# Kernel optimization log

Hardware: AMD Instinct MI355X
Metric: run time of the kernel (lower is better)

Reference implementation:

```python
import jax, jax.numpy as jnp
import numpy as np
from functools import partial

INPUT_DIM = 256
HIDDEN = 512
NUM_LAYERS = 2

def _linp(key, fan_in, shape):
    # torch nn.Linear/Conv default init: U(-1/sqrt(fan_in), 1/sqrt(fan_in))
    bound = 1.0 / np.sqrt(fan_in)
    return jax.random.uniform(key, shape, jnp.float32, -bound, bound)

def setup_inputs() -> dict:
    key = jax.random.key(0)
    ks = iter(jax.random.split(key, 64))
    d = {}
    d["x"] = jax.random.normal(next(ks), (32, 16, 1, 64, 64), jnp.float32)
    # encoder convs (OIHW)
    d["conv1_w"] = _linp(next(ks), 1 * 9, (16, 1, 3, 3));   d["conv1_b"] = _linp(next(ks), 1 * 9, (16,))
    d["conv2_w"] = _linp(next(ks), 16 * 9, (32, 16, 3, 3)); d["conv2_b"] = _linp(next(ks), 16 * 9, (32,))
    d["conv3_w"] = _linp(next(ks), 32 * 9, (INPUT_DIM, 32, 3, 3)); d["conv3_b"] = _linp(next(ks), 32 * 9, (INPUT_DIM,))
    # LSTM cells: per layer 4 gate linears (forget, input, cell, output), in = input+hidden
    for j in range(NUM_LAYERS):
        fan = (INPUT_DIM if j == 0 else HIDDEN) + HIDDEN
        for g in ("f", "i", "g", "o"):
            d[f"W{g}{j}"] = _linp(next(ks), fan, (fan, HIDDEN))
            d[f"b{g}{j}"] = _linp(next(ks), fan, (HIDDEN,))
    # classifier
    d["cw1"] = _linp(next(ks), HIDDEN, (HIDDEN, 128)); d["cb1"] = _linp(next(ks), HIDDEN, (128,))
    d["cw2"] = _linp(next(ks), 128, (128, 64));        d["cb2"] = _linp(next(ks), 128, (64,))
    d["cw3"] = _linp(next(ks), 64, (64, 6));           d["cb3"] = _linp(next(ks), 64, (6,))
    return d

def _conv(x, w, b):
    y = jax.lax.conv_general_dilated(x, w, (1, 1), "SAME",
                                     dimension_numbers=("NCHW", "OIHW", "NCHW"))
    return y + b[None, :, None, None]

def _maxpool2(x):
    return jax.lax.reduce_window(x, -jnp.inf, jax.lax.max,
                                 (1, 1, 2, 2), (1, 1, 2, 2), "VALID")

def reference(x, conv1_w, conv1_b, conv2_w, conv2_b, conv3_w, conv3_b,
              Wf0, bf0, Wi0, bi0, Wg0, bg0, Wo0, bo0,
              Wf1, bf1, Wi1, bi1, Wg1, bg1, Wo1, bo1,
              cw1, cb1, cw2, cb2, cw3, cb3):
    B, T, C, H, W = x.shape
    xf = x.reshape(B * T, C, H, W)
    h = _maxpool2(jax.nn.relu(_conv(xf, conv1_w, conv1_b)))
    h = _maxpool2(jax.nn.relu(_conv(h, conv2_w, conv2_b)))
    h = jax.nn.relu(_conv(h, conv3_w, conv3_b))
    emb = h.mean(axis=(2, 3)).reshape(B, T, -1)  # AdaptiveAvgPool2d((1,1)); dropout = identity (eval)

    layers = [(Wf0, bf0, Wi0, bi0, Wg0, bg0, Wo0, bo0),
              (Wf1, bf1, Wi1, bi1, Wg1, bg1, Wo1, bo1)]

    def step(carry, x_t):
        hs, cs = carry
        inp = x_t
        new_h, new_c = [], []
        for j, (Wf, bf, Wi, bi, Wg, bg, Wo, bo) in enumerate(layers):
            comb = jnp.concatenate([inp, hs[j]], axis=1)  # [B, in+H]
            f_t = jax.nn.sigmoid(comb @ Wf + bf)
            i_t = jax.nn.sigmoid(comb @ Wi + bi)
            g_t = jnp.tanh(comb @ Wg + bg)
            o_t = jax.nn.sigmoid(comb @ Wo + bo)
            c_n = f_t * cs[j] + i_t * g_t
            h_n = o_t * jnp.tanh(c_n)
            new_h.append(h_n); new_c.append(c_n)
            inp = h_n
        return (tuple(new_h), tuple(new_c)), None

    h0 = tuple(jnp.zeros((B, HIDDEN), x.dtype) for _ in range(NUM_LAYERS))
    c0 = tuple(jnp.zeros((B, HIDDEN), x.dtype) for _ in range(NUM_LAYERS))
    (hs, _), _ = jax.lax.scan(step, (h0, c0), jnp.swapaxes(emb, 0, 1))
    last = hs[-1]  # [B, HIDDEN], last timestep top-layer h (dropout = identity)

    y = jax.nn.relu(last @ cw1 + cb1)
    y = jax.nn.relu(y @ cw2 + cb2)
    return y @ cw3 + cb3  # [B, 6]
```

## Files before the change

kernel.cpp:

```cpp
#include <hip/hip_runtime.h>
#include <math.h>

__global__ void k_conv1(const float* __restrict__ x, const float* __restrict__ w,
                        const float* __restrict__ bias, float* __restrict__ out) {
  int idx = blockIdx.x * 256 + threadIdx.x;
  int ox = idx & 31, oy = (idx >> 5) & 31, oc = (idx >> 10) & 15, n = idx >> 14;
  const float* im = x + n * 4096;
  float wv[9];
#pragma unroll
  for (int i = 0; i < 9; ++i) wv[i] = w[oc * 9 + i];
  float bs = bias[oc];
  float m = 0.f;
#pragma unroll
  for (int dy = 0; dy < 2; ++dy)
#pragma unroll
    for (int dx = 0; dx < 2; ++dx) {
      int cy = oy * 2 + dy, cx = ox * 2 + dx;
      float s = bs;
#pragma unroll
      for (int ky = 0; ky < 3; ++ky) {
        int yy = cy + ky - 1;
        if (yy < 0 || yy >= 64) continue;
#pragma unroll
        for (int kx = 0; kx < 3; ++kx) {
          int xx = cx + kx - 1;
          if (xx < 0 || xx >= 64) continue;
          s += im[yy * 64 + xx] * wv[ky * 3 + kx];
        }
      }
      m = fmaxf(m, fmaxf(s, 0.f));
    }
  out[idx] = m;
}

__global__ void k_prep_w(const float* __restrict__ w2, float* __restrict__ w2t,
                         const float* __restrict__ w3, float* __restrict__ w3t) {
  int id = blockIdx.x * 256 + threadIdx.x;
  if (id < 73728) {
    int ct = id >> 8, oc = id & 255;
    int c = ct / 9, tap = ct - 9 * c;
    w3t[id] = w3[(oc * 32 + c) * 9 + tap];
  }
  if (id < 4608) {
    int ct = id >> 5, oc = id & 31;
    int c = ct / 9, tap = ct - 9 * c;
    w2t[id] = w2[(oc * 16 + c) * 9 + tap];
  }
}

__global__ __launch_bounds__(256) void k_conv2(
    const float* __restrict__ a1, const float* __restrict__ w2t,
    const float* __restrict__ bias, float* __restrict__ a2) {
  __shared__ __align__(16) float ins[8 * 1024];
  int n = blockIdx.x, ocg = blockIdx.y;
  int tid = threadIdx.x;
  int py = tid >> 4, px = tid & 15;
  int y0 = 2 * py - 1, x0 = 2 * px - 1;
  float acc[16][4] = {};
  const float* wb = w2t + ocg * 16;
  for (int ph = 0; ph < 2; ++ph) {
    __syncthreads();
    const float4* src = (const float4*)(a1 + n * 16384 + ph * 8192);
    for (int i = tid; i < 2048; i += 256) ((float4*)ins)[i] = src[i];
    __syncthreads();
    for (int c = 0; c < 8; ++c) {
      float wv[4][4];
#pragma unroll
      for (int r = 0; r < 4; ++r) {
        int y = y0 + r;
        bool vy = (y >= 0) && (y < 32);
        int yc = vy ? y : 0;
#pragma unroll
        for (int cc = 0; cc < 4; ++cc) {
          int xx = x0 + cc;
          bool vx = (xx >= 0) && (xx < 32);
          int xc = vx ? xx : 0;
          float t = ins[c * 1024 + yc * 32 + xc];
          wv[r][cc] = (vy && vx) ? t : 0.f;
        }
      }
      int ch = ph * 8 + c;
#pragma unroll
      for (int ky = 0; ky < 3; ++ky)
#pragma unroll
        for (int kx = 0; kx < 3; ++kx) {
          const float* w16 = wb + (ch * 9 + ky * 3 + kx) * 32;
#pragma unroll
          for (int i = 0; i < 4; ++i) {
            float vv = wv[(i >> 1) + ky][(i & 1) + kx];
#pragma unroll
            for (int j = 0; j < 16; ++j) acc[j][i] += vv * w16[j];
          }
        }
    }
  }
  const float* bp = bias + ocg * 16;
  float4 o[4];
#pragma unroll
  for (int j = 0; j < 16; ++j) {
    float m = fmaxf(fmaxf(acc[j][0], acc[j][1]), fmaxf(acc[j][2], acc[j][3]));
    ((float*)o)[j] = fmaxf(m + bp[j], 0.f);
  }
  float4* dst = (float4*)(a2 + (size_t)(n * 256 + tid) * 32 + ocg * 16);
#pragma unroll
  for (int q = 0; q < 4; ++q) dst[q] = o[q];
}

__global__ __launch_bounds__(512) void k_conv3(
    const float* __restrict__ a2, const float* __restrict__ w3t,
    const float* __restrict__ bias, float* __restrict__ comb0) {
  __shared__ __align__(16) float ins[324 * 20];
  float4* ins4 = (float4*)ins;
  int n = blockIdx.x, ocb = blockIdx.y;
  int tid = threadIdx.x;
  for (int i = tid; i < 1620; i += 512) ins4[i] = float4{0.f, 0.f, 0.f, 0.f};
  int wvid = __builtin_amdgcn_readfirstlane(tid >> 6);
  int lane = tid & 63;
  int tr = lane >> 4, tc = lane & 15;
  float acc[4][8] = {};
  const float* wbase = w3t + ocb * 64 + wvid * 8;
  const float4* src = (const float4*)(a2 + (size_t)n * 8192);
  for (int hf = 0; hf < 2; ++hf) {
    __syncthreads();
    for (int i = tid; i < 1024; i += 512) {
      int px = i >> 2, cg = i & 3;
      int p = ((px >> 4) + 1) * 18 + (px & 15) + 1;
      ins4[p * 5 + (cg ^ ((p >> 3) & 3))] = src[px * 8 + hf * 4 + cg];
    }
    __syncthreads();
    for (int cg = 0; cg < 4; ++cg) {
      int chb = hf * 16 + cg * 4;
#pragma unroll
      for (int dr = 0; dr < 6; ++dr) {
#pragma unroll
        for (int dc = 0; dc < 3; ++dc) {
          int pp = (4 * tr + dr) * 18 + tc + dc;
          float4 v = ins4[pp * 5 + (cg ^ ((pp >> 3) & 3))];
#pragma unroll
          for (int c = 0; c < 4; ++c) {
            float vv = ((const float*)&v)[c];
            const int ilo = (dr - 2 < 0) ? 0 : dr - 2;
            const int ihi = (dr < 3) ? dr : 3;
#pragma unroll
            for (int i = ilo; i <= ihi; ++i) {
              const float* w8 = wbase + (((chb + c) * 9 + (dr - i) * 3 + dc) * 256);
#pragma unroll
              for (int j = 0; j < 8; ++j) acc[i][j] += vv * w8[j];
            }
          }
        }
      }
    }
  }
  const float* bp = bias + ocb * 64 + wvid * 8;
  int bb = n >> 4, tt = n & 15;
#pragma unroll
  for (int j = 0; j < 8; ++j) {
    float bj = bp[j];
    float s = 0.f;
#pragma unroll
    for (int i = 0; i < 4; ++i) s += fmaxf(acc[i][j] + bj, 0.f);
#pragma unroll
    for (int off = 32; off; off >>= 1) s += __shfl_down(s, off, 64);
    if (lane == 0) {
      int oc = ocb * 64 + wvid * 8 + j;
      comb0[(size_t)(tt * 768 + oc) * 32 + bb] = s * (1.f / 256.f);
    }
  }
}

struct TPtrs { const float* in[8]; float* out[8]; };

__global__ void k_transpose(TPtrs p) {
  __shared__ float tile[32][33];
  int z = blockIdx.z;
  int fan = (z < 4) ? 768 : 1024;
  int k0 = blockIdx.x * 32, h0 = blockIdx.y * 32;
  if (k0 >= fan) return;
  const float* in = p.in[z];
  float* out = p.out[z];
  int tx = threadIdx.x, ty = threadIdx.y;
  for (int r = 0; r < 32; r += 8)
    tile[ty + r][tx] = in[(k0 + ty + r) * 512 + h0 + tx];
  __syncthreads();
  for (int r = 0; r < 32; r += 8)
    out[(h0 + ty + r) * fan + k0 + tx] = tile[tx][ty + r];
}

template <int IN>
__global__ __launch_bounds__(512) void k_lstm(
    const float* __restrict__ comb,
    float* __restrict__ houtA, float* __restrict__ houtB,
    float* __restrict__ cT,
    const float* __restrict__ WfT, const float* __restrict__ WiT,
    const float* __restrict__ WgT, const float* __restrict__ WoT,
    const float* __restrict__ bf, const float* __restrict__ bi,
    const float* __restrict__ bg, const float* __restrict__ bo) {
  constexpr int FAN = IN + 512;
  constexpr int PR = FAN + 4;
  constexpr int KT = FAN / 16;
  __shared__ __align__(16) float wl[4 * PR];
  __shared__ __align__(16) float gsum[4][16][36];
  __shared__ float pre[4][33];
  const int tid = threadIdx.x;
  const int h = blockIdx.x;
  if (tid < FAN / 4) {
    ((float4*)(wl + 0 * PR))[tid] = ((const float4*)(WfT + h * FAN))[tid];
    ((float4*)(wl + 1 * PR))[tid] = ((const float4*)(WiT + h * FAN))[tid];
    ((float4*)(wl + 2 * PR))[tid] = ((const float4*)(WgT + h * FAN))[tid];
    ((float4*)(wl + 3 * PR))[tid] = ((const float4*)(WoT + h * FAN))[tid];
  }
  __syncthreads();
  const int kq = tid >> 5, c = (tid >> 3) & 3, bq = tid & 7;
  const int kbase = kq * KT;
  const float4* w4 = (const float4*)(wl + c * PR + kbase);
  const float4* a4 = (const float4*)comb + bq;
  float acc0 = 0.f, acc1 = 0.f, acc2 = 0.f, acc3 = 0.f;
#pragma unroll
  for (int kk = 0; kk < KT / 4; ++kk) {
    float4 w = w4[kk];
#pragma unroll
    for (int j = 0; j < 4; ++j) {
      float wj = ((const float*)&w)[j];
      float4 a = a4[(size_t)(kbase + kk * 4 + j) * 8];
      acc0 += wj * a.x; acc1 += wj * a.y; acc2 += wj * a.z; acc3 += wj * a.w;
    }
  }
  ((float4*)&gsum[c][kq][0])[bq] = float4{acc0, acc1, acc2, acc3};
  __syncthreads();
  if (tid < 128) {
    int cc = tid >> 5, b = tid & 31;
    float s = 0.f;
#pragma unroll
    for (int q = 0; q < 16; ++q) s += gsum[cc][q][b];
    pre[cc][b] = s;
  }
  __syncthreads();
  if (tid < 32) {
    int b = tid;
    float fp = pre[0][b] + bf[h];
    float ip = pre[1][b] + bi[h];
    float gp = pre[2][b] + bg[h];
    float op = pre[3][b] + bo[h];
    float ft = 1.f / (1.f + expf(-fp));
    float it = 1.f / (1.f + expf(-ip));
    float gt = tanhf(gp);
    float ot = 1.f / (1.f + expf(-op));
    float cn = ft * cT[h * 32 + b] + it * gt;
    cT[h * 32 + b] = cn;
    float hn = ot * tanhf(cn);
    houtA[h * 32 + b] = hn;
    houtB[h * 32 + b] = hn;
  }
}

__global__ void k_cls(const float* __restrict__ h1T, const float* __restrict__ cw1,
                      const float* __restrict__ cb1, const float* __restrict__ cw2,
                      const float* __restrict__ cb2, const float* __restrict__ cw3,
                      const float* __restrict__ cb3, float* __restrict__ out) {
  __shared__ float hv[512];
  __shared__ float y1[128];
  __shared__ float y2[64];
  int b = blockIdx.x, tid = threadIdx.x;
  for (int i = tid; i < 512; i += 128) hv[i] = h1T[i * 32 + b];
  __syncthreads();
  float s = cb1[tid];
  for (int k = 0; k < 512; ++k) s += hv[k] * cw1[k * 128 + tid];
  y1[tid] = fmaxf(s, 0.f);
  __syncthreads();
  if (tid < 64) {
    float s2 = cb2[tid];
    for (int k = 0; k < 128; ++k) s2 += y1[k] * cw2[k * 64 + tid];
    y2[tid] = fmaxf(s2, 0.f);
  }
  __syncthreads();
  if (tid < 6) {
    float s3 = cb3[tid];
    for (int k = 0; k < 64; ++k) s3 += y2[k] * cw3[k * 6 + tid];
    out[b * 6 + tid] = s3;
  }
}

extern "C" void kernel_launch(void* const* d_in, const int* in_sizes, int n_in,
                              void* d_out, int out_size, void* d_ws, size_t ws_size,
                              hipStream_t stream) {
  const float* x  = (const float*)d_in[0];
  const float* w1 = (const float*)d_in[1];
  const float* b1 = (const float*)d_in[2];
  const float* w2 = (const float*)d_in[3];
  const float* b2 = (const float*)d_in[4];
  const float* w3 = (const float*)d_in[5];
  const float* b3 = (const float*)d_in[6];
  const float* cw1 = (const float*)d_in[23];
  const float* cb1 = (const float*)d_in[24];
  const float* cw2 = (const float*)d_in[25];
  const float* cb2 = (const float*)d_in[26];
  const float* cw3 = (const float*)d_in[27];
  const float* cb3 = (const float*)d_in[28];

  float* ws = (float*)d_ws;
  float* a1    = ws;
  float* wt    = ws;
  float* comb0 = ws + 3670016;
  float* comb1 = ws + 4087808;
  float* c0    = ws + 4644864;
  float* c1    = ws + 4661248;
  float* a2    = ws + 8388608;
  float* w2t   = ws + 12582912;
  float* w3t   = ws + 12587520;
  const int C0 = 768 * 32, C1 = 1024 * 32;

  k_prep_w<<<288, 256, 0, stream>>>(w2, w2t, w3, w3t);
  k_conv1<<<32768, 256, 0, stream>>>(x, w1, b1, a1);
  k_conv2<<<dim3(512, 2), 256, 0, stream>>>(a1, w2t, b2, a2);

  hipMemsetAsync(comb0 + 256 * 32, 0, (size_t)512 * 32 * 4, stream);
  hipMemsetAsync(comb1 + 512 * 32, 0, (size_t)512 * 32 * 4, stream);
  hipMemsetAsync(c0, 0, (size_t)2 * 512 * 32 * 4, stream);

  k_conv3<<<dim3(512, 4), 512, 0, stream>>>(a2, w3t, b3, comb0);

  TPtrs tp;
  for (int g = 0; g < 4; ++g) {
    tp.in[g]      = (const float*)d_in[7 + 2 * g];
    tp.out[g]     = wt + g * (512 * 768);
    tp.in[4 + g]  = (const float*)d_in[15 + 2 * g];
    tp.out[4 + g] = wt + 4 * (512 * 768) + g * (512 * 1024);
  }
  k_transpose<<<dim3(32, 16, 8), dim3(32, 8), 0, stream>>>(tp);

  const float* wl0[4] = {wt, wt + 393216, wt + 786432, wt + 1179648};
  float* l1base = wt + 1572864;
  const float* wl1[4] = {l1base, l1base + 524288, l1base + 1048576, l1base + 1572864};

  for (int t = 0; t < 16; ++t) {
    k_lstm<256><<<512, 512, 0, stream>>>(
        comb0 + (size_t)t * C0,
        comb0 + (size_t)(t + 1) * C0 + 256 * 32,
        comb1 + (size_t)t * C1,
        c0, wl0[0], wl0[1], wl0[2], wl0[3],
        (const float*)d_in[8], (const float*)d_in[10],
        (const float*)d_in[12], (const float*)d_in[14]);
    k_lstm<512><<<512, 512, 0, stream>>>(
        comb1 + (size_t)t * C1,
        comb1 + (size_t)(t + 1) * C1 + 512 * 32,
        comb1 + (size_t)(t + 1) * C1 + 512 * 32,
        c1, wl1[0], wl1[1], wl1[2], wl1[3],
        (const float*)d_in[16], (const float*)d_in[18],
        (const float*)d_in[20], (const float*)d_in[22]);
  }

  k_cls<<<32, 128, 0, stream>>>(comb1 + (size_t)16 * C1 + 512 * 32,
                                cw1, cb1, cw2, cb2, cw3, cb3, (float*)d_out);
}
```

Before: 673.5 us.

## Wavefront-pipeline LSTM layers into paired launches and widen conv3 output tile

The LSTM time loop is restructured as a wavefront: layer 0 at step t+1 and layer 1 at step t run in a single 1024-block launch. This replaces 32 serial launches with 17 and lets the two layers' work overlap. The thread-to-(gate,k) mapping inside the LSTM body is also changed. Separately, conv3 now computes 16 output channels per wave instead of 8 over half the grid, with a min-occupancy launch bound, and drops the XOR swizzle on the shared input tile. The wider conv3 tile raises register pressure, and removing the swizzle may bring back LDS bank conflicts.

```diff
diff --git a/kernel.cpp b/kernel.cpp
--- a/kernel.cpp
+++ b/kernel.cpp
@@ -106,7 +106,7 @@
   for (int q = 0; q < 4; ++q) dst[q] = o[q];
 }
 
-__global__ __launch_bounds__(512) void k_conv3(
+__global__ __launch_bounds__(512, 4) void k_conv3(
     const float* __restrict__ a2, const float* __restrict__ w3t,
     const float* __restrict__ bias, float* __restrict__ comb0) {
   __shared__ __align__(16) float ins[324 * 20];
@@ -117,15 +117,15 @@
   int wvid = __builtin_amdgcn_readfirstlane(tid >> 6);
   int lane = tid & 63;
   int tr = lane >> 4, tc = lane & 15;
-  float acc[4][8] = {};
-  const float* wbase = w3t + ocb * 64 + wvid * 8;
+  float acc[4][16] = {};
+  const float* wbase = w3t + ocb * 128 + wvid * 16;
   const float4* src = (const float4*)(a2 + (size_t)n * 8192);
   for (int hf = 0; hf < 2; ++hf) {
     __syncthreads();
     for (int i = tid; i < 1024; i += 512) {
       int px = i >> 2, cg = i & 3;
       int p = ((px >> 4) + 1) * 18 + (px & 15) + 1;
-      ins4[p * 5 + (cg ^ ((p >> 3) & 3))] = src[px * 8 + hf * 4 + cg];
+      ins4[p * 5 + cg] = src[px * 8 + hf * 4 + cg];
     }
     __syncthreads();
     for (int cg = 0; cg < 4; ++cg) {
@@ -135,7 +135,7 @@
 #pragma unroll
         for (int dc = 0; dc < 3; ++dc) {
           int pp = (4 * tr + dr) * 18 + tc + dc;
-          float4 v = ins4[pp * 5 + (cg ^ ((pp >> 3) & 3))];
+          float4 v = ins4[pp * 5 + cg];
 #pragma unroll
           for (int c = 0; c < 4; ++c) {
             float vv = ((const float*)&v)[c];
@@ -143,19 +143,19 @@
             const int ihi = (dr < 3) ? dr : 3;
 #pragma unroll
             for (int i = ilo; i <= ihi; ++i) {
-              const float* w8 = wbase + (((chb + c) * 9 + (dr - i) * 3 + dc) * 256);
-#pragma unroll
-              for (int j = 0; j < 8; ++j) acc[i][j] += vv * w8[j];
+              const float* w16 = wbase + (((chb + c) * 9 + (dr - i) * 3 + dc) * 256);
+#pragma unroll
+              for (int j = 0; j < 16; ++j) acc[i][j] += vv * w16[j];
             }
           }
         }
       }
     }
   }
-  const float* bp = bias + ocb * 64 + wvid * 8;
+  const float* bp = bias + ocb * 128 + wvid * 16;
   int bb = n >> 4, tt = n & 15;
 #pragma unroll
-  for (int j = 0; j < 8; ++j) {
+  for (int j = 0; j < 16; ++j) {
     float bj = bp[j];
     float s = 0.f;
 #pragma unroll
@@ -163,7 +163,7 @@
 #pragma unroll
     for (int off = 32; off; off >>= 1) s += __shfl_down(s, off, 64);
     if (lane == 0) {
-      int oc = ocb * 64 + wvid * 8 + j;
+      int oc = ocb * 128 + wvid * 16 + j;
       comb0[(size_t)(tt * 768 + oc) * 32 + bb] = s * (1.f / 256.f);
     }
   }
@@ -187,34 +187,29 @@
     out[(h0 + ty + r) * fan + k0 + tx] = tile[tx][ty + r];
 }
 
+struct LstmArgs {
+  const float* comb; float* houtA; float* houtB; float* cT;
+  const float* Wf; const float* Wi; const float* Wg; const float* Wo;
+  const float* bf; const float* bi; const float* bg; const float* bo;
+};
+
 template <int IN>
-__global__ __launch_bounds__(512) void k_lstm(
-    const float* __restrict__ comb,
-    float* __restrict__ houtA, float* __restrict__ houtB,
-    float* __restrict__ cT,
-    const float* __restrict__ WfT, const float* __restrict__ WiT,
-    const float* __restrict__ WgT, const float* __restrict__ WoT,
-    const float* __restrict__ bf, const float* __restrict__ bi,
-    const float* __restrict__ bg, const float* __restrict__ bo) {
+__device__ __forceinline__ void lstm_body(int h, int tid, const LstmArgs& A,
+                                          float* wl, float* gsum, float* pre) {
   constexpr int FAN = IN + 512;
   constexpr int PR = FAN + 4;
   constexpr int KT = FAN / 16;
-  __shared__ __align__(16) float wl[4 * PR];
-  __shared__ __align__(16) float gsum[4][16][36];
-  __shared__ float pre[4][33];
-  const int tid = threadIdx.x;
-  const int h = blockIdx.x;
   if (tid < FAN / 4) {
-    ((float4*)(wl + 0 * PR))[tid] = ((const float4*)(WfT + h * FAN))[tid];
-    ((float4*)(wl + 1 * PR))[tid] = ((const float4*)(WiT + h * FAN))[tid];
-    ((float4*)(wl + 2 * PR))[tid] = ((const float4*)(WgT + h * FAN))[tid];
-    ((float4*)(wl + 3 * PR))[tid] = ((const float4*)(WoT + h * FAN))[tid];
-  }
-  __syncthreads();
-  const int kq = tid >> 5, c = (tid >> 3) & 3, bq = tid & 7;
+    ((float4*)(wl + 0 * PR))[tid] = ((const float4*)(A.Wf + (size_t)h * FAN))[tid];
+    ((float4*)(wl + 1 * PR))[tid] = ((const float4*)(A.Wi + (size_t)h * FAN))[tid];
+    ((float4*)(wl + 2 * PR))[tid] = ((const float4*)(A.Wg + (size_t)h * FAN))[tid];
+    ((float4*)(wl + 3 * PR))[tid] = ((const float4*)(A.Wo + (size_t)h * FAN))[tid];
+  }
+  __syncthreads();
+  const int kq = (tid >> 3) & 15, c = tid >> 7, bq = tid & 7;
   const int kbase = kq * KT;
   const float4* w4 = (const float4*)(wl + c * PR + kbase);
-  const float4* a4 = (const float4*)comb + bq;
+  const float4* a4 = (const float4*)A.comb + bq;
   float acc0 = 0.f, acc1 = 0.f, acc2 = 0.f, acc3 = 0.f;
 #pragma unroll
   for (int kk = 0; kk < KT / 4; ++kk) {
@@ -226,32 +221,50 @@
       acc0 += wj * a.x; acc1 += wj * a.y; acc2 += wj * a.z; acc3 += wj * a.w;
     }
   }
-  ((float4*)&gsum[c][kq][0])[bq] = float4{acc0, acc1, acc2, acc3};
+  ((float4*)(gsum + (c * 16 + kq) * 36))[bq] = float4{acc0, acc1, acc2, acc3};
   __syncthreads();
   if (tid < 128) {
     int cc = tid >> 5, b = tid & 31;
     float s = 0.f;
 #pragma unroll
-    for (int q = 0; q < 16; ++q) s += gsum[cc][q][b];
-    pre[cc][b] = s;
+    for (int q = 0; q < 16; ++q) s += gsum[(cc * 16 + q) * 36 + b];
+    pre[cc * 33 + b] = s;
   }
   __syncthreads();
   if (tid < 32) {
     int b = tid;
-    float fp = pre[0][b] + bf[h];
-    float ip = pre[1][b] + bi[h];
-    float gp = pre[2][b] + bg[h];
-    float op = pre[3][b] + bo[h];
+    float fp = pre[0 * 33 + b] + A.bf[h];
+    float ip = pre[1 * 33 + b] + A.bi[h];
+    float gp = pre[2 * 33 + b] + A.bg[h];
+    float op = pre[3 * 33 + b] + A.bo[h];
     float ft = 1.f / (1.f + expf(-fp));
     float it = 1.f / (1.f + expf(-ip));
     float gt = tanhf(gp);
     float ot = 1.f / (1.f + expf(-op));
-    float cn = ft * cT[h * 32 + b] + it * gt;
-    cT[h * 32 + b] = cn;
+    float cn = ft * A.cT[h * 32 + b] + it * gt;
+    A.cT[h * 32 + b] = cn;
     float hn = ot * tanhf(cn);
-    houtA[h * 32 + b] = hn;
-    houtB[h * 32 + b] = hn;
-  }
+    A.houtA[h * 32 + b] = hn;
+    A.houtB[h * 32 + b] = hn;
+  }
+}
+
+template <int IN>
+__global__ __launch_bounds__(512) void k_lstm(LstmArgs a) {
+  __shared__ __align__(16) float wl[4 * 1028];
+  __shared__ __align__(16) float gsum[4 * 16 * 36];
+  __shared__ float pre[4 * 33];
+  lstm_body<IN>(blockIdx.x, threadIdx.x, a, wl, gsum, pre);
+}
+
+__global__ __launch_bounds__(512) void k_lstm_pair(LstmArgs a0, LstmArgs a1) {
+  __shared__ __align__(16) float wl[4 * 1028];
+  __shared__ __align__(16) float gsum[4 * 16 * 36];
+  __shared__ float pre[4 * 33];
+  if (blockIdx.x < 512)
+    lstm_body<256>(blockIdx.x, threadIdx.x, a0, wl, gsum, pre);
+  else
+    lstm_body<512>(blockIdx.x - 512, threadIdx.x, a1, wl, gsum, pre);
 }
 
 __global__ void k_cls(const float* __restrict__ h1T, const float* __restrict__ cw1,
@@ -318,7 +331,7 @@
   hipMemsetAsync(comb1 + 512 * 32, 0, (size_t)512 * 32 * 4, stream);
   hipMemsetAsync(c0, 0, (size_t)2 * 512 * 32 * 4, stream);
 
-  k_conv3<<<dim3(512, 4), 512, 0, stream>>>(a2, w3t, b3, comb0);
+  k_conv3<<<dim3(512, 2), 512, 0, stream>>>(a2, w3t, b3, comb0);
 
   TPtrs tp;
   for (int g = 0; g < 4; ++g) {
@@ -333,22 +346,33 @@
   float* l1base = wt + 1572864;
   const float* wl1[4] = {l1base, l1base + 524288, l1base + 1048576, l1base + 1572864};
 
-  for (int t = 0; t < 16; ++t) {
-    k_lstm<256><<<512, 512, 0, stream>>>(
-        comb0 + (size_t)t * C0,
-        comb0 + (size_t)(t + 1) * C0 + 256 * 32,
-        comb1 + (size_t)t * C1,
-        c0, wl0[0], wl0[1], wl0[2], wl0[3],
-        (const float*)d_in[8], (const float*)d_in[10],
-        (const float*)d_in[12], (const float*)d_in[14]);
-    k_lstm<512><<<512, 512, 0, stream>>>(
-        comb1 + (size_t)t * C1,
-        comb1 + (size_t)(t + 1) * C1 + 512 * 32,
-        comb1 + (size_t)(t + 1) * C1 + 512 * 32,
-        c1, wl1[0], wl1[1], wl1[2], wl1[3],
-        (const float*)d_in[16], (const float*)d_in[18],
-        (const float*)d_in[20], (const float*)d_in[22]);
-  }
+  auto L0 = [&](int t) {
+    LstmArgs a;
+    a.comb = comb0 + (size_t)t * C0;
+    a.houtA = comb0 + (size_t)(t + 1) * C0 + 256 * 32;
+    a.houtB = comb1 + (size_t)t * C1;
+    a.cT = c0;
+    a.Wf = wl0[0]; a.Wi = wl0[1]; a.Wg = wl0[2]; a.Wo = wl0[3];
+    a.bf = (const float*)d_in[8];  a.bi = (const float*)d_in[10];
+    a.bg = (const float*)d_in[12]; a.bo = (const float*)d_in[14];
+    return a;
+  };
+  auto L1 = [&](int t) {
+    LstmArgs a;
+    a.comb = comb1 + (size_t)t * C1;
+    a.houtA = comb1 + (size_t)(t + 1) * C1 + 512 * 32;
+    a.houtB = a.houtA;
+    a.cT = c1;
+    a.Wf = wl1[0]; a.Wi = wl1[1]; a.Wg = wl1[2]; a.Wo = wl1[3];
+    a.bf = (const float*)d_in[16]; a.bi = (const float*)d_in[18];
+    a.bg = (const float*)d_in[20]; a.bo = (const float*)d_in[22];
+    return a;
+  };
+
+  k_lstm<256><<<512, 512, 0, stream>>>(L0(0));
+  for (int p = 0; p < 15; ++p)
+    k_lstm_pair<<<1024, 512, 0, stream>>>(L0(p + 1), L1(p));
+  k_lstm<512><<<512, 512, 0, stream>>>(L1(15));
 
   k_cls<<<32, 128, 0, stream>>>(comb1 + (size_t)16 * C1 + 512 * 32,
                                 cw1, cb1, cw2, cb2, cw3, cb3, (float*)d_out);
```

New measurement: 687.6 us. 1.02x slower.
